# Kernel tuning notes

Hardware: AMD Instinct MI355X
Metric: run time of the kernel (lower is better)

The kernel has to match this reference:

```python
import jax, jax.numpy as jnp
import numpy as np

EPS = 1e-5

@jax.custom_vjp
def sign_ste(x):
    # binarize to {-1, +1}; sign(0) maps to +1 as in most binary-net impls
    return jnp.where(x >= 0, 1.0, -1.0).astype(x.dtype)

def _sign_fwd(x):
    return sign_ste(x), x

def _sign_bwd(x, g):
    # straight-through estimator with hardtanh clipping
    return (g * (jnp.abs(x) <= 1.0).astype(g.dtype),)

sign_ste.defvjp(_sign_fwd, _sign_bwd)


def setup_inputs() -> dict:
    key = jax.random.key(0)
    k1, k2, k3 = jax.random.split(key, 3)
    N, Cin, Cout = 65536, 1024, 1024
    return {
        "x": jax.random.normal(k1, (N, Cin), dtype=jnp.float32),
        "gamma": jnp.ones((Cin,), dtype=jnp.float32),
        "beta": jnp.zeros((Cin,), dtype=jnp.float32),
        "W": jax.random.normal(k2, (Cout, Cin), dtype=jnp.float32) * 0.03,
        "b": jnp.zeros((Cout,), dtype=jnp.float32),
        "scale": jnp.ones((Cout,), dtype=jnp.float32),
        "alpha": jnp.float32(0.25),
    }


def reference(x, gamma, beta, W, b, scale, alpha):
    # 1) BatchNorm1d centering (training-mode batch statistics over nodes)
    mu = jnp.mean(x, axis=0)
    var = jnp.var(x, axis=0)
    xh = (x - mu) * jax.lax.rsqrt(var + EPS) * gamma + beta
    # 2) STE binarize activations
    xq = sign_ste(xh)
    # 3) binary linear: sign(W) GEMM + bias  -> [N, Cout]
    wq = sign_ste(W)
    y = jnp.einsum('nc,oc->no', xq, wq) + b
    # 4) learned per-channel rescale
    y = y * scale
    # 5) PReLU
    return jnp.where(y > 0, y, alpha * y)
```

## Files before the change

kernel.cpp:

```cpp
#include <hip/hip_runtime.h>
#include <stdint.h>
#include <math.h>

#define NROWS 65536
#define CIN   1024
#define COUT  1024
#define BN_EPS 1e-5


static constexpr size_t OFF_PSUM = 0;
static constexpr size_t OFF_PSQ  = 2u * 1024 * 1024;
static constexpr size_t OFF_MU   = 4u * 1024 * 1024;
static constexpr size_t OFF_INV  = 4u * 1024 * 1024 + 4096;
static constexpr size_t OFF_WB   = 5u * 1024 * 1024;
static constexpr size_t OFF_AB   = 6u * 1024 * 1024;

typedef uint64_t u64x2 __attribute__((ext_vector_type(2)));
typedef uint32_t u32x4 __attribute__((ext_vector_type(4)));
typedef const u32x4 __attribute__((address_space(4)))* c4p;

__global__ __launch_bounds__(256) void k_stats_partial(
    const float* __restrict__ x, double* __restrict__ psum, double* __restrict__ psq) {
  int tid = threadIdx.x;
  size_t r0 = (size_t)blockIdx.x * 256;
  const float4* xp = (const float4*)x + r0 * 256 + tid;
  double s0 = 0, s1 = 0, s2 = 0, s3 = 0;
  double q0 = 0, q1 = 0, q2 = 0, q3 = 0;
  for (int r = 0; r < 256; r += 8) {
    float4 v[8];
#pragma unroll
    for (int u = 0; u < 8; ++u) v[u] = xp[(size_t)(r + u) * 256];
#pragma unroll
    for (int u = 0; u < 8; ++u) {
      double a = (double)v[u].x, b = (double)v[u].y;
      double c = (double)v[u].z, d = (double)v[u].w;
      s0 += a; q0 = fma(a, a, q0);
      s1 += b; q1 = fma(b, b, q1);
      s2 += c; q2 = fma(c, c, q2);
      s3 += d; q3 = fma(d, d, q3);
    }
  }
  size_t base = (size_t)blockIdx.x * CIN + (size_t)tid * 4;
  double2* ps = (double2*)(psum + base);
  ps[0] = make_double2(s0, s1);
  ps[1] = make_double2(s2, s3);
  double2* pq = (double2*)(psq + base);
  pq[0] = make_double2(q0, q1);
  pq[1] = make_double2(q2, q3);
}

__global__ __launch_bounds__(256) void k_stats_final(
    const double* __restrict__ psum, const double* __restrict__ psq,
    float* __restrict__ mu, float* __restrict__ inv) {
  __shared__ double sd[4][64];
  __shared__ double sq[4][64];
  int tid = threadIdx.x, lane = tid & 63, g = tid >> 6;
  int col = blockIdx.x * 64 + lane;
  double s = 0, q = 0;
  for (int i = 0; i < 64; ++i) {
    size_t chunk = (size_t)(g * 64 + i);
    s += psum[chunk * CIN + col];
    q += psq [chunk * CIN + col];
  }
  sd[g][lane] = s;
  sq[g][lane] = q;
  __syncthreads();
  if (g == 0) {
    s = sd[0][lane] + sd[1][lane] + sd[2][lane] + sd[3][lane];
    q = sq[0][lane] + sq[1][lane] + sq[2][lane] + sq[3][lane];
    double mean = s / (double)NROWS;
    double var  = q / (double)NROWS - mean * mean;
    mu[col]  = (float)mean;
    inv[col] = (float)(1.0 / sqrt(var + (double)BN_EPS));
  }
}

__global__ __launch_bounds__(256) void k_binarize_x(
    const float* __restrict__ x, const float* __restrict__ mu,
    const float* __restrict__ inv, const float* __restrict__ gamma,
    const float* __restrict__ beta, uint64_t* __restrict__ Abits) {
  int tid = threadIdx.x, lane = tid & 63, wv = tid >> 6;
  float4 M  = ((const float4*)mu)[tid];
  float4 I  = ((const float4*)inv)[tid];
  float4 G  = ((const float4*)gamma)[tid];
  float4 Bt = ((const float4*)beta)[tid];
  size_t n0 = (size_t)blockIdx.x * 8;
  const float4* xp = (const float4*)x + n0 * 256 + tid;
  for (int r = 0; r < 8; ++r) {
    float4 v = xp[(size_t)r * 256];
    float h0 = ((v.x - M.x) * I.x) * G.x + Bt.x;
    float h1 = ((v.y - M.y) * I.y) * G.y + Bt.y;
    float h2 = ((v.z - M.z) * I.z) * G.z + Bt.z;
    float h3 = ((v.w - M.w) * I.w) * G.w + Bt.w;
    uint64_t b0 = __ballot(h0 >= 0.0f);
    uint64_t b1 = __ballot(h1 >= 0.0f);
    uint64_t b2 = __ballot(h2 >= 0.0f);
    uint64_t b3 = __ballot(h3 >= 0.0f);
    uint64_t t0 = b0, t1 = b1;
    if (lane == 1) { t0 = b2; t1 = b3; }
    if (lane < 2) {
      u64x2 val; val.x = t0; val.y = t1;
      *(u64x2*)(Abits + (n0 + r) * 16 + wv * 4 + lane * 2) = val;
    }
  }
}

__global__ __launch_bounds__(256) void k_binarize_w(
    const float* __restrict__ W, uint64_t* __restrict__ Wbits) {
  int tid = threadIdx.x, lane = tid & 63, wv = tid >> 6;
  size_t o0 = (size_t)blockIdx.x * 8;
  const float4* wp = (const float4*)W + o0 * 256 + tid;
  for (int r = 0; r < 8; ++r) {
    float4 v = wp[(size_t)r * 256];
    uint64_t b0 = __ballot(v.x >= 0.0f);
    uint64_t b1 = __ballot(v.y >= 0.0f);
    uint64_t b2 = __ballot(v.z >= 0.0f);
    uint64_t b3 = __ballot(v.w >= 0.0f);
    uint64_t t0 = b0, t1 = b1;
    if (lane == 1) { t0 = b2; t1 = b3; }
    if (lane < 2) {
      u64x2 val; val.x = t0; val.y = t1;
      *(u64x2*)(Wbits + (o0 + r) * 16 + wv * 4 + lane * 2) = val;
    }
  }
}

__global__ __launch_bounds__(256) void k_bingemm(
    const uint32_t* __restrict__ Abits, const uint32_t* __restrict__ Wbits,
    const float* __restrict__ bias, const float* __restrict__ scale,
    const float* __restrict__ alphaPtr, float* __restrict__ out) {
  int tid = threadIdx.x;
  int o = blockIdx.x * 256 + tid;

  u32x4 B[8];
  const u32x4* wp = (const u32x4*)(Wbits + (size_t)o * 32);
#pragma unroll
  for (int j = 0; j < 8; ++j) B[j] = wp[j];

  float alpha = alphaPtr[0];
  float sc = scale[o];
  float c2 = -2.0f * sc;
  float c1 = (1024.0f + bias[o]) * sc;

  size_t n0 = (size_t)blockIdx.y * 64;
  c4p Ar = (c4p)(uintptr_t)(Abits + n0 * 32);
  float* op = out + n0 * COUT + o;

  for (int r = 0; r < 64; ++r) {
    int d0 = 0, d1 = 0, d2 = 0, d3 = 0;
#pragma unroll
    for (int j = 0; j < 8; ++j) {
      u32x4 a = Ar[j];
      d0 += __builtin_popcount(a.x ^ B[j].x);
      d1 += __builtin_popcount(a.y ^ B[j].y);
      d2 += __builtin_popcount(a.z ^ B[j].z);
      d3 += __builtin_popcount(a.w ^ B[j].w);
    }
    Ar += 8;
    int d = (d0 + d1) + (d2 + d3);
    float y = fmaf((float)d, c2, c1);
    *op = y > 0.0f ? y : alpha * y;
    op += COUT;
  }
}

extern "C" void kernel_launch(void* const* d_in, const int* in_sizes, int n_in,
                              void* d_out, int out_size, void* d_ws, size_t ws_size,
                              hipStream_t stream) {
  const float* x     = (const float*)d_in[0];
  const float* gamma = (const float*)d_in[1];
  const float* beta  = (const float*)d_in[2];
  const float* W     = (const float*)d_in[3];
  const float* b     = (const float*)d_in[4];
  const float* scale = (const float*)d_in[5];
  const float* alpha = (const float*)d_in[6];
  float* out = (float*)d_out;

  char* ws = (char*)d_ws;
  double*   psum  = (double*)(ws + OFF_PSUM);
  double*   psq   = (double*)(ws + OFF_PSQ);
  float*    mu    = (float*)(ws + OFF_MU);
  float*    inv   = (float*)(ws + OFF_INV);
  uint64_t* Wbits = (uint64_t*)(ws + OFF_WB);
  uint64_t* Abits = (uint64_t*)(ws + OFF_AB);

  k_stats_partial<<<dim3(NROWS / 256), 256, 0, stream>>>(x, psum, psq);
  k_stats_final<<<dim3(CIN / 64), 256, 0, stream>>>(psum, psq, mu, inv);
  k_binarize_w<<<dim3(COUT / 8), 256, 0, stream>>>(W, Wbits);
  k_binarize_x<<<dim3(NROWS / 8), 256, 0, stream>>>(x, mu, inv, gamma, beta, Abits);
  k_bingemm<<<dim3(COUT / 256, NROWS / 64), 256, 0, stream>>>(
      (const uint32_t*)Abits, (const uint32_t*)Wbits, b, scale, alpha, out);
}
```

Before: 607.4 us.

## Stage binary activation tile in LDS and rebalance stats kernels

The GEMM kernel now copies a 128-row tile of packed activation bits into shared memory and reads it from LDS. Before, every thread read the same rows through scalar constant-address loads. Rows per block double, so the W-bit register setup is amortized over more rows. The stats partial kernel uses 128-row chunks, giving twice as many blocks, and the final reduction is regridded to 16 columns per block. The workspace offsets are enlarged to fit the bigger partial-sum buffers. The risk is extra LDS traffic and a barrier in the GEMM. The LDS reads are broadcasts, which may be slower than the scalar loads they replace.

```diff
diff --git a/kernel.cpp b/kernel.cpp
--- a/kernel.cpp
+++ b/kernel.cpp
@@ -9,24 +9,23 @@
 
 
 static constexpr size_t OFF_PSUM = 0;
-static constexpr size_t OFF_PSQ  = 2u * 1024 * 1024;
-static constexpr size_t OFF_MU   = 4u * 1024 * 1024;
-static constexpr size_t OFF_INV  = 4u * 1024 * 1024 + 4096;
-static constexpr size_t OFF_WB   = 5u * 1024 * 1024;
-static constexpr size_t OFF_AB   = 6u * 1024 * 1024;
+static constexpr size_t OFF_PSQ  = 4ull * 1024 * 1024;
+static constexpr size_t OFF_MU   = 8ull * 1024 * 1024;
+static constexpr size_t OFF_INV  = 8ull * 1024 * 1024 + 4096;
+static constexpr size_t OFF_WB   = 9ull * 1024 * 1024;
+static constexpr size_t OFF_AB   = 10ull * 1024 * 1024;
 
 typedef uint64_t u64x2 __attribute__((ext_vector_type(2)));
 typedef uint32_t u32x4 __attribute__((ext_vector_type(4)));
-typedef const u32x4 __attribute__((address_space(4)))* c4p;
 
 __global__ __launch_bounds__(256) void k_stats_partial(
     const float* __restrict__ x, double* __restrict__ psum, double* __restrict__ psq) {
   int tid = threadIdx.x;
-  size_t r0 = (size_t)blockIdx.x * 256;
+  size_t r0 = (size_t)blockIdx.x * 128;
   const float4* xp = (const float4*)x + r0 * 256 + tid;
   double s0 = 0, s1 = 0, s2 = 0, s3 = 0;
   double q0 = 0, q1 = 0, q2 = 0, q3 = 0;
-  for (int r = 0; r < 256; r += 8) {
+  for (int r = 0; r < 128; r += 8) {
     float4 v[8];
 #pragma unroll
     for (int u = 0; u < 8; ++u) v[u] = xp[(size_t)(r + u) * 256];
@@ -52,26 +51,30 @@
 __global__ __launch_bounds__(256) void k_stats_final(
     const double* __restrict__ psum, const double* __restrict__ psq,
     float* __restrict__ mu, float* __restrict__ inv) {
-  __shared__ double sd[4][64];
-  __shared__ double sq[4][64];
-  int tid = threadIdx.x, lane = tid & 63, g = tid >> 6;
-  int col = blockIdx.x * 64 + lane;
+  __shared__ double sd[16][16];
+  __shared__ double sq[16][16];
+  int tid = threadIdx.x;
+  int cl = tid & 15;
+  int g  = tid >> 4;
+  int col = blockIdx.x * 16 + cl;
   double s = 0, q = 0;
-  for (int i = 0; i < 64; ++i) {
-    size_t chunk = (size_t)(g * 64 + i);
+  for (int i = 0; i < 32; ++i) {
+    size_t chunk = (size_t)(g * 32 + i);
     s += psum[chunk * CIN + col];
     q += psq [chunk * CIN + col];
   }
-  sd[g][lane] = s;
-  sq[g][lane] = q;
+  sd[g][cl] = s;
+  sq[g][cl] = q;
   __syncthreads();
-  if (g == 0) {
-    s = sd[0][lane] + sd[1][lane] + sd[2][lane] + sd[3][lane];
-    q = sq[0][lane] + sq[1][lane] + sq[2][lane] + sq[3][lane];
+  if (tid < 16) {
+    s = 0; q = 0;
+#pragma unroll
+    for (int i = 0; i < 16; ++i) { s += sd[i][tid]; q += sq[i][tid]; }
     double mean = s / (double)NROWS;
     double var  = q / (double)NROWS - mean * mean;
-    mu[col]  = (float)mean;
-    inv[col] = (float)(1.0 / sqrt(var + (double)BN_EPS));
+    int c = blockIdx.x * 16 + tid;
+    mu[c]  = (float)mean;
+    inv[c] = (float)(1.0 / sqrt(var + (double)BN_EPS));
   }
 }
 
@@ -125,12 +128,22 @@
   }
 }
 
+#define K5_ROWS 128
 __global__ __launch_bounds__(256) void k_bingemm(
     const uint32_t* __restrict__ Abits, const uint32_t* __restrict__ Wbits,
     const float* __restrict__ bias, const float* __restrict__ scale,
     const float* __restrict__ alphaPtr, float* __restrict__ out) {
+  __shared__ uint32_t tile[K5_ROWS * 32];
   int tid = threadIdx.x;
   int o = blockIdx.x * 256 + tid;
+  size_t n0 = (size_t)blockIdx.y * K5_ROWS;
+
+  {
+    const u32x4* src = (const u32x4*)(Abits + n0 * 32);
+    u32x4* dst = (u32x4*)tile;
+#pragma unroll
+    for (int i = 0; i < 4; ++i) dst[i * 256 + tid] = src[i * 256 + tid];
+  }
 
   u32x4 B[8];
   const u32x4* wp = (const u32x4*)(Wbits + (size_t)o * 32);
@@ -142,21 +155,20 @@
   float c2 = -2.0f * sc;
   float c1 = (1024.0f + bias[o]) * sc;
 
-  size_t n0 = (size_t)blockIdx.y * 64;
-  c4p Ar = (c4p)(uintptr_t)(Abits + n0 * 32);
+  __syncthreads();
+
   float* op = out + n0 * COUT + o;
-
-  for (int r = 0; r < 64; ++r) {
+  for (int r = 0; r < K5_ROWS; ++r) {
+    const u32x4* A = (const u32x4*)(tile + r * 32);
     int d0 = 0, d1 = 0, d2 = 0, d3 = 0;
 #pragma unroll
     for (int j = 0; j < 8; ++j) {
-      u32x4 a = Ar[j];
+      u32x4 a = A[j];
       d0 += __builtin_popcount(a.x ^ B[j].x);
       d1 += __builtin_popcount(a.y ^ B[j].y);
       d2 += __builtin_popcount(a.z ^ B[j].z);
       d3 += __builtin_popcount(a.w ^ B[j].w);
     }
-    Ar += 8;
     int d = (d0 + d1) + (d2 + d3);
     float y = fmaf((float)d, c2, c1);
     *op = y > 0.0f ? y : alpha * y;
@@ -184,10 +196,10 @@
   uint64_t* Wbits = (uint64_t*)(ws + OFF_WB);
   uint64_t* Abits = (uint64_t*)(ws + OFF_AB);
 
-  k_stats_partial<<<dim3(NROWS / 256), 256, 0, stream>>>(x, psum, psq);
-  k_stats_final<<<dim3(CIN / 64), 256, 0, stream>>>(psum, psq, mu, inv);
+  k_stats_partial<<<dim3(NROWS / 128), 256, 0, stream>>>(x, psum, psq);
+  k_stats_final<<<dim3(CIN / 16), 256, 0, stream>>>(psum, psq, mu, inv);
   k_binarize_w<<<dim3(COUT / 8), 256, 0, stream>>>(W, Wbits);
   k_binarize_x<<<dim3(NROWS / 8), 256, 0, stream>>>(x, mu, inv, gamma, beta, Abits);
-  k_bingemm<<<dim3(COUT / 256, NROWS / 64), 256, 0, stream>>>(
+  k_bingemm<<<dim3(COUT / 256, NROWS / K5_ROWS), 256, 0, stream>>>(
       (const uint32_t*)Abits, (const uint32_t*)Wbits, b, scale, alpha, out);
 }
```

Measured after the change: 591.5 us. -2.6%, faster.
